# Optimization experiments

Measured on AMD Instinct MI355X. Metric: run time of the kernel, lower is better.

## Reference

```python
import jax, jax.numpy as jnp
import numpy as np

SCALES = [1.0, 0.9, 0.8, 0.7, 0.6]  # [1 - i/10 for i in range(level=5)]
RES_SCALE = 1.0


def conv2d(x, w, b, pad):
    # NCHW conv, OIHW weights, stride 1, symmetric padding
    y = jax.lax.conv_general_dilated(
        x, w, window_strides=(1, 1), padding=[(pad, pad), (pad, pad)],
        dimension_numbers=("NCHW", "OIHW", "NCHW"))
    return y + b[None, :, None, None]


def _cubic_kernel(d, a=-0.75):
    # torch-style bicubic kernel (a = -0.75)
    d = jnp.abs(d)
    w1 = ((a + 2.0) * d - (a + 3.0)) * d * d + 1.0          # |d| <= 1
    w2 = (((a * d) - 5.0 * a) * d + 8.0 * a) * d - 4.0 * a  # 1 < |d| < 2
    return jnp.where(d <= 1.0, w1, jnp.where(d < 2.0, w2, 0.0))


def _resize_axis(x, out_size, axis):
    in_size = x.shape[axis]
    scale = in_size / out_size
    src = (jnp.arange(out_size, dtype=jnp.float32) + 0.5) * scale - 0.5  # align_corners=False
    x0 = jnp.floor(src)
    t = src - x0
    x0 = x0.astype(jnp.int32)
    out = 0.0
    bshape = [1] * x.ndim
    bshape[axis] = out_size
    for off in range(-1, 3):
        idx = jnp.clip(x0 + off, 0, in_size - 1)  # border replicate
        wgt = _cubic_kernel(t - off).reshape(bshape)
        out = out + jnp.take(x, idx, axis=axis) * wgt
    return out


def bicubic(x, oh, ow):
    return _resize_axis(_resize_axis(x, oh, 2), ow, 3)


def setup_inputs() -> dict:
    key = jax.random.key(0)
    ks = jax.random.split(key, 7)
    C, Cr = 64, 32  # channel=64, reduction=2
    x = jax.random.normal(ks[0], (4, C, 48, 48), dtype=jnp.float32)
    wb = jax.random.normal(ks[1], (Cr, C, 3, 3), dtype=jnp.float32) * 0.05  # conv_match_L_base
    bb = jax.random.normal(ks[2], (Cr,), dtype=jnp.float32) * 0.05
    wm = jax.random.normal(ks[3], (Cr, C, 3, 3), dtype=jnp.float32) * 0.05  # conv_match
    bm = jax.random.normal(ks[4], (Cr,), dtype=jnp.float32) * 0.05
    wa = jax.random.normal(ks[5], (C, C, 1, 1), dtype=jnp.float32) * 0.05   # conv_assembly
    ba = jax.random.normal(ks[6], (C,), dtype=jnp.float32) * 0.05
    return {"x": x, "wb": wb, "bb": bb, "wm": wm, "bm": bm, "wa": wa, "ba": ba}


def reference(x, wb, bb, wm, bm, wa, ba):
    N, C, H, W = x.shape
    mb = conv2d(x, wb, bb, 1)                           # [N,Cr,H,W]
    Cr = mb.shape[1]
    mb = mb.reshape(N, Cr, H * W).transpose(0, 2, 1)    # [N,HW,Cr]  (queries)
    raws, keys = [], []
    for s in SCALES:
        ref = x if s == 1.0 else bicubic(x, int(H * s), int(W * s))
        raws.append(conv2d(ref, wa, ba, 0).reshape(N, C, -1))   # values [N,C,HiWi]
        keys.append(conv2d(ref, wm, bm, 1).reshape(N, Cr, -1))  # keys   [N,Cr,HiWi]
    pyr = jnp.concatenate(keys, axis=-1)                        # [N,Cr,L]
    raw = jnp.concatenate(raws, axis=-1).transpose(0, 2, 1)     # [N,L,C]
    score = jax.nn.softmax(jnp.einsum("nqc,ncl->nql", mb, pyr), axis=-1)  # [N,HW,L]
    y = jnp.einsum("nql,nlc->nqc", score, raw)                  # [N,HW,C]
    y = y.transpose(0, 2, 1).reshape(N, C, H, W)
    return y * RES_SCALE + x
```

## Files before the change

### kernel.cpp

```cpp
#include <hip/hip_runtime.h>
#include <math.h>

typedef unsigned short ushort_t;
typedef __attribute__((ext_vector_type(8))) short short8;
typedef __attribute__((ext_vector_type(4))) float float4v;

#define NB 4
#define C 64
#define CR 32
#define HW 2304
#define LTOT 7470
#define LPAD 7472
#define NSEG 15
#define SEG 512
#define LOG2E 1.44269504088896f

#define YP_F 0
#define LP_F 8847360
#define MBBF_F   8985600
#define KEYBF_F  9133056
#define RAWTBF_F 9611136
#define WPK_F    10567552
#define WPQ_F    10576768
#define WPV_F    10585984

static __device__ __forceinline__ ushort_t f2bf(float f) {
  union { float f; unsigned u; } v; v.f = f;
  unsigned r = v.u + 0x7FFF + ((v.u >> 16) & 1);
  return (ushort_t)(r >> 16);
}

__device__ __forceinline__ float cubicw(float d) {
  float ad = fabsf(d);
  float w1 = (1.25f * ad - 2.25f) * ad * ad + 1.0f;
  float w2 = ((-0.75f * ad + 3.75f) * ad - 6.0f) * ad + 3.0f;
  return ad <= 1.0f ? w1 : (ad < 2.0f ? w2 : 0.0f);
}

__global__ void k_zero(ushort_t* __restrict__ xt) {
  int i = blockIdx.x * 256 + threadIdx.x;
  if (i < 264000) {
    uint4 z = {0u, 0u, 0u, 0u};
    *(uint4*)(xt + (size_t)i * 8) = z;
  }
}

__global__ __launch_bounds__(256) void k_pad0(const float* __restrict__ x,
                                              ushort_t* __restrict__ xt) {
  __shared__ float tile[64][49];
  int py = blockIdx.x, n = blockIdx.y, t = threadIdx.x;
#pragma unroll
  for (int i = 0; i < 12; i++) {
    int idx = i * 256 + t;
    int c = idx / 48, px = idx % 48;
    tile[c][px] = x[(size_t)(n * 64 + c) * HW + py * 48 + px];
  }
  __syncthreads();
#pragma unroll
  for (int i = 0; i < 12; i++) {
    int idx = i * 256 + t;
    int c = idx & 63, px = idx >> 6;
    xt[(size_t)(n * 2500 + (py + 1) * 50 + px + 1) * 64 + c] = f2bf(tile[c][px]);
  }
}

__global__ void k_resize(const float* __restrict__ x, ushort_t* __restrict__ xt) {
  int tid = blockIdx.x * 256 + threadIdx.x;
  int D, Dp, PDD, rem, pixb;
  if (tid < 473344)       { D = 43; Dp = 45; PDD = 2025; rem = tid;           pixb = 10000; }
  else if (tid < 843008)  { D = 38; Dp = 40; PDD = 1600; rem = tid - 473344;  pixb = 18100; }
  else if (tid < 1121792) { D = 33; Dp = 35; PDD = 1225; rem = tid - 843008;  pixb = 24500; }
  else                    { D = 28; Dp = 30; PDD = 900;  rem = tid - 1121792; pixb = 29400; }
  int DD = D * D;
  int pix = rem % DD, nc = rem / DD;
  int py = pix / D, px = pix % D;
  float scale = 48.0f / (float)D;
  float sy = ((float)py + 0.5f) * scale - 0.5f;
  float sx = ((float)px + 0.5f) * scale - 0.5f;
  float y0f = floorf(sy), x0f = floorf(sx);
  int y0 = (int)y0f, x0 = (int)x0f;
  float ty = sy - y0f, tx = sx - x0f;
  float wy[4], wxv[4];
#pragma unroll
  for (int k = 0; k < 4; k++) {
    wy[k]  = cubicw(ty - (float)(k - 1));
    wxv[k] = cubicw(tx - (float)(k - 1));
  }
  const float* src = x + (size_t)nc * HW;
  float acc = 0.f;
#pragma unroll
  for (int dy = 0; dy < 4; ++dy) {
    int iy = min(max(y0 - 1 + dy, 0), 47);
    const float* row = src + iy * 48;
    float a = 0.f;
#pragma unroll
    for (int dx = 0; dx < 4; ++dx) {
      int ix = min(max(x0 - 1 + dx, 0), 47);
      a = fmaf(wxv[dx], row[ix], a);
    }
    acc = fmaf(wy[dy], a, acc);
  }
  int n = nc >> 6, c = nc & 63;
  xt[(size_t)(pixb + n * PDD + (py + 1) * Dp + (px + 1)) * 64 + c] = f2bf(acc);
}

__global__ void k_wpack(const float* __restrict__ wm, const float* __restrict__ wb,
                        const float* __restrict__ wa, ushort_t* __restrict__ wpk,
                        ushort_t* __restrict__ wpq, ushort_t* __restrict__ wpv) {
  int tid = blockIdx.x * 256 + threadIdx.x;
  if (tid >= 5120) return;
  int lane = tid & 63, col = lane & 15, kg = lane >> 4;
  if (tid < 4608) {
    int f = (tid >> 6) % 36;
    bool isq = tid >= 2304;
    int tap = f >> 2, half = (f >> 1) & 1, crt = f & 1;
    int cr = crt * 16 + col;
    int ic0 = half * 32 + kg * 8;
    const float* w = isq ? wb : wm;
    short8 v;
#pragma unroll
    for (int j = 0; j < 8; j++) v[j] = (short)f2bf(w[cr * 576 + (ic0 + j) * 9 + tap]);
    *(short8*)((isq ? wpq : wpk) + (size_t)f * 512 + lane * 8) = v;
  } else {
    int id = tid - 4608;
    int f = id >> 6;
    int half = f >> 2, vt = f & 3;
    int c = vt * 16 + col, ic0 = half * 32 + kg * 8;
    short8 v;
#pragma unroll
    for (int j = 0; j < 8; j++) v[j] = (short)f2bf(wa[c * 64 + ic0 + j]);
    *(short8*)(wpv + (size_t)f * 512 + lane * 8) = v;
  }
}

__global__ __launch_bounds__(256) void k_conv(const ushort_t* __restrict__ xt,
    const ushort_t* __restrict__ wpk, const ushort_t* __restrict__ wpq,
    const ushort_t* __restrict__ wpv, const float* __restrict__ bm,
    const float* __restrict__ bb, const float* __restrict__ ba,
    ushort_t* __restrict__ keybf, ushort_t* __restrict__ mbbf,
    ushort_t* __restrict__ rawtbf) {
  int t = threadIdx.x;
  int unit = blockIdx.x * 4 + (t >> 6);
  if (unit >= 938) return;
  int lane = t & 63, col = lane & 15, quad = lane >> 4;
  int n = blockIdx.y;
  int tile = unit >> 1, crt = unit & 1;
  int D, Dp, PDD, DD, pixb, lb, tloc;
  if (tile < 144)      { D = 48; Dp = 50; PDD = 2500; DD = 2304; pixb = 0;     lb = 0;    tloc = tile; }
  else if (tile < 260) { D = 43; Dp = 45; PDD = 2025; DD = 1849; pixb = 10000; lb = 2304; tloc = tile - 144; }
  else if (tile < 351) { D = 38; Dp = 40; PDD = 1600; DD = 1444; pixb = 18100; lb = 4153; tloc = tile - 260; }
  else if (tile < 420) { D = 33; Dp = 35; PDD = 1225; DD = 1089; pixb = 24500; lb = 5597; tloc = tile - 351; }
  else                 { D = 28; Dp = 30; PDD = 900;  DD = 784;  pixb = 29400; lb = 6686; tloc = tile - 420; }
  bool lvl0 = (tile < 144);

  int p = tloc * 16 + col;
  int pv = min(p, DD - 1);
  int py = pv / D, px = pv - py * D;
  const ushort_t* xb = xt + ((size_t)(pixb + n * PDD + (py + 1) * Dp + (px + 1))) * 64 + quad * 8;

  float4v Dk = {0.f, 0.f, 0.f, 0.f};
  float4v Dq = {0.f, 0.f, 0.f, 0.f};
  float4v Dv0 = {0.f, 0.f, 0.f, 0.f};
  float4v Dv1 = {0.f, 0.f, 0.f, 0.f};

#pragma unroll
  for (int dy = -1; dy <= 1; dy++) {
#pragma unroll
    for (int dx = -1; dx <= 1; dx++) {
      int tap = (dy + 1) * 3 + (dx + 1);
      const ushort_t* ab = xb + (dy * Dp + dx) * 64;
#pragma unroll
      for (int half = 0; half < 2; half++) {
        short8 A = *(const short8*)(ab + half * 32);
        int f = (tap * 2 + half) * 2 + crt;
        short8 Bk = *(const short8*)(wpk + (size_t)f * 512 + lane * 8);
        Dk = __builtin_amdgcn_mfma_f32_16x16x32_bf16(A, Bk, Dk, 0, 0, 0);
        if (lvl0) {
          short8 Bq = *(const short8*)(wpq + (size_t)f * 512 + lane * 8);
          Dq = __builtin_amdgcn_mfma_f32_16x16x32_bf16(A, Bq, Dq, 0, 0, 0);
        }
        if (tap == 4) {
          short8 Bv0 = *(const short8*)(wpv + (size_t)(half * 4 + crt * 2) * 512 + lane * 8);
          short8 Bv1 = *(const short8*)(wpv + (size_t)(half * 4 + crt * 2 + 1) * 512 + lane * 8);
          Dv0 = __builtin_amdgcn_mfma_f32_16x16x32_bf16(A, Bv0, Dv0, 0, 0, 0);
          Dv1 = __builtin_amdgcn_mfma_f32_16x16x32_bf16(A, Bv1, Dv1, 0, 0, 0);
        }
      }
    }
  }

  float biask = bm[crt * 16 + col];
  float biasq = bb[crt * 16 + col];
  float biasv0 = ba[crt * 32 + col];
  float biasv1 = ba[crt * 32 + 16 + col];
  int prow = tloc * 16 + quad * 4;
#pragma unroll
  for (int r = 0; r < 4; r++) {
    if (prow + r < DD) {
      int l = lb + prow + r;
      keybf[(size_t)(n * LTOT + l) * 32 + crt * 16 + col] = f2bf(Dk[r] + biask);
      if (lvl0) mbbf[(size_t)(n * HW + l) * 32 + crt * 16 + col] = f2bf((Dq[r] + biasq) * LOG2E);
      rawtbf[(size_t)(n * 64 + crt * 32 + col) * LPAD + l] = f2bf(Dv0[r] + biasv0);
      rawtbf[(size_t)(n * 64 + crt * 32 + 16 + col) * LPAD + l] = f2bf(Dv1[r] + biasv1);
    }
  }
}

__global__ __launch_bounds__(256, 4) void k_attn(const ushort_t* __restrict__ mb,
    const ushort_t* __restrict__ keyb, const ushort_t* __restrict__ rawt,
    float* __restrict__ Yp, float* __restrict__ lp) {
  __shared__ __align__(16) ushort_t VsF[2][4096];
  __shared__ __align__(16) ushort_t Pq[4][32 * 72];

  int t = threadIdx.x;
  int n = blockIdx.y, seg = blockIdx.z;
  int lane = t & 63, wv = t >> 6;
  int col = lane & 15, quad = lane >> 4;
  int qb = blockIdx.x * 128 + wv * 32;
  int l_begin = seg * SEG;
  int l_end = min(l_begin + SEG, LTOT);
  int nfull = (l_end - l_begin) >> 6;
  int rem = (l_end - l_begin) & 63;
  int nch = nfull + (rem ? 1 : 0);

  const ushort_t* keyn = keyb + (size_t)n * LTOT * CR;
  const ushort_t* rawn = rawt + (size_t)n * C * LPAD;

  short8 qA0 = *(const short8*)(mb + ((size_t)(n * HW + qb + col)) * CR + quad * 8);
  short8 qA1 = *(const short8*)(mb + ((size_t)(n * HW + qb + 16 + col)) * CR + quad * 8);

  int ct0 = (t >> 6) & 3, g0 = (t >> 4) & 3, cc0 = t & 15;
  size_t so0 = (size_t)(ct0 * 16 + cc0) * LPAD + g0 * 8;

  float4v Y0[4], Y1[4];
#pragma unroll
  for (int ct = 0; ct < 4; ct++)
#pragma unroll
    for (int r = 0; r < 4; r++) { Y0[ct][r] = 0.f; Y1[ct][r] = 0.f; }
  float ls0 = 0.f, ls1 = 0.f;
  const float4v zero4 = {0.f, 0.f, 0.f, 0.f};
  ushort_t* Pw = Pq[wv];

  uint4 va = *(const uint4*)(rawn + so0 + l_begin);
  uint4 vb = *(const uint4*)(rawn + so0 + 32 + l_begin);
  int buf = 0;

  for (int ch = 0; ch < nch; ++ch) {
    int l0 = l_begin + ch * 64;
    *(uint4*)&VsF[buf][t * 8] = va;
    *(uint4*)&VsF[buf][(t + 256) * 8] = vb;
    if (ch + 1 < nch) {
      int ln = l0 + 64;
      va = *(const uint4*)(rawn + so0 + ln);
      vb = *(const uint4*)(rawn + so0 + 32 + ln);
    }
    __syncthreads();

    bool tail = (rem != 0) && (ch == nfull);
#pragma unroll
    for (int tt = 0; tt < 4; tt++) {
      short8 kf = *(const short8*)(keyn + (size_t)(l0 + tt * 16 + col) * CR + quad * 8);
      float4v S0 = __builtin_amdgcn_mfma_f32_16x16x32_bf16(kf, qA0, zero4, 0, 0, 0);
      float4v S1 = __builtin_amdgcn_mfma_f32_16x16x32_bf16(kf, qA1, zero4, 0, 0, 0);
      int lbase = tt * 16 + quad * 4;
      float p0[4], p1[4];
#pragma unroll
      for (int r = 0; r < 4; r++) {
        bool ok = !tail || (lbase + r < rem);
        float a = __builtin_amdgcn_exp2f(S0[r]);
        float b = __builtin_amdgcn_exp2f(S1[r]);
        p0[r] = ok ? a : 0.f;
        p1[r] = ok ? b : 0.f;
        ls0 += p0[r];
        ls1 += p1[r];
      }
      union { float f; unsigned u; } c0, c1;
      uint2 w;
      c0.f = p0[0]; c1.f = p0[1];
      w.x = ((c0.u + 0x8000u) >> 16) | ((c1.u + 0x8000u) & 0xFFFF0000u);
      c0.f = p0[2]; c1.f = p0[3];
      w.y = ((c0.u + 0x8000u) >> 16) | ((c1.u + 0x8000u) & 0xFFFF0000u);
      *(uint2*)&Pw[col * 72 + lbase] = w;
      c0.f = p1[0]; c1.f = p1[1];
      w.x = ((c0.u + 0x8000u) >> 16) | ((c1.u + 0x8000u) & 0xFFFF0000u);
      c0.f = p1[2]; c1.f = p1[3];
      w.y = ((c0.u + 0x8000u) >> 16) | ((c1.u + 0x8000u) & 0xFFFF0000u);
      *(uint2*)&Pw[(16 + col) * 72 + lbase] = w;
    }

#pragma unroll
    for (int kt = 0; kt < 2; kt++) {
      short8 a0 = *(const short8*)&Pw[col * 72 + kt * 32 + quad * 8];
      short8 a1 = *(const short8*)&Pw[(16 + col) * 72 + kt * 32 + quad * 8];
#pragma unroll
      for (int ct = 0; ct < 4; ct++) {
        short8 bV = *(const short8*)&VsF[buf][(((kt << 2) | ct) * 64 + lane) * 8];
        Y0[ct] = __builtin_amdgcn_mfma_f32_16x16x32_bf16(a0, bV, Y0[ct], 0, 0, 0);
        Y1[ct] = __builtin_amdgcn_mfma_f32_16x16x32_bf16(a1, bV, Y1[ct], 0, 0, 0);
      }
    }
    buf ^= 1;
  }

  ls0 += __shfl_xor(ls0, 16); ls0 += __shfl_xor(ls0, 32);
  ls1 += __shfl_xor(ls1, 16); ls1 += __shfl_xor(ls1, 32);

  float* yo = Yp + ((size_t)(seg * NB + n) * HW + qb) * C;
#pragma unroll
  for (int ct = 0; ct < 4; ct++)
#pragma unroll
    for (int r = 0; r < 4; r++) {
      yo[(quad * 4 + r) * C + ct * 16 + col] = Y0[ct][r];
      yo[(16 + quad * 4 + r) * C + ct * 16 + col] = Y1[ct][r];
    }
  if (quad == 0) {
    int base = (seg * NB + n) * HW + qb;
    lp[base + col] = ls0;
    lp[base + 16 + col] = ls1;
  }
}

__global__ void k_combine(const float* __restrict__ x, const float* __restrict__ ws,
                          float* __restrict__ out) {
  int tid = blockIdx.x * 256 + threadIdx.x;
  int c = tid & 63;
  int t2 = tid >> 6;
  int q = t2 % HW;
  int n = t2 / HW;
  const float* Yv = ws + YP_F;
  const float* lpv = ws + LP_F;
  int i0 = n * HW + q;
  float den = 0.f, num = 0.f;
#pragma unroll
  for (int s = 0; s < NSEG; s++) {
    int idx = s * NB * HW + i0;
    den += lpv[idx];
    num += Yv[(size_t)idx * C + c];
  }
  int oi = (n * C + c) * HW + q;
  out[oi] = num / den + x[oi];
}

extern "C" void kernel_launch(void* const* d_in, const int* in_sizes, int n_in,
                              void* d_out, int out_size, void* d_ws, size_t ws_size,
                              hipStream_t stream) {
  const float* x  = (const float*)d_in[0];
  const float* wb = (const float*)d_in[1];
  const float* bb = (const float*)d_in[2];
  const float* wm = (const float*)d_in[3];
  const float* bm = (const float*)d_in[4];
  const float* wa = (const float*)d_in[5];
  const float* ba = (const float*)d_in[6];
  float* out = (float*)d_out;
  float* ws = (float*)d_ws;
  ushort_t* xt     = (ushort_t*)ws;
  ushort_t* mbbf   = (ushort_t*)(ws + MBBF_F);
  ushort_t* keybf  = (ushort_t*)(ws + KEYBF_F);
  ushort_t* rawtbf = (ushort_t*)(ws + RAWTBF_F);
  ushort_t* wpk    = (ushort_t*)(ws + WPK_F);
  ushort_t* wpq    = (ushort_t*)(ws + WPQ_F);
  ushort_t* wpv    = (ushort_t*)(ws + WPV_F);

  k_zero<<<1032, 256, 0, stream>>>(xt);
  k_pad0<<<dim3(48, 4), 256, 0, stream>>>(x, xt);
  k_resize<<<5166, 256, 0, stream>>>(x, xt);
  k_wpack<<<20, 256, 0, stream>>>(wm, wb, wa, wpk, wpq, wpv);
  k_conv<<<dim3(235, 4), 256, 0, stream>>>(xt, wpk, wpq, wpv, bm, bb, ba,
                                           keybf, mbbf, rawtbf);
  k_attn<<<dim3(18, 4, NSEG), 256, 0, stream>>>(mbbf, keybf, rawtbf,
      ws + YP_F, ws + LP_F);
  k_combine<<<2304, 256, 0, stream>>>(x, ws, out);
}
```

Before: 154.1 us.

## Merge prep kernels and fuse split-L combine into attention via counter

Folds the zero, pad, resize and weight-pack kernels into one prep launch. The prep kernel zeroes only the padding border instead of the whole buffer. The separate combine kernel is removed: each attention block increments a per-(n, query-tile) atomic counter, and the last segment block to arrive reduces the partial outputs and writes the final result with the residual. This cuts launch count and a full zero pass, at the cost of threadfence/atomic ordering and a serial tail in the last-arriving blocks.

```diff
diff --git a/kernel.cpp b/kernel.cpp
--- a/kernel.cpp
+++ b/kernel.cpp
@@ -23,6 +23,7 @@
 #define WPK_F    10567552
 #define WPQ_F    10576768
 #define WPV_F    10585984
+#define CNT_F    10588032
 
 static __device__ __forceinline__ ushort_t f2bf(float f) {
   union { float f; unsigned u; } v; v.f = f;
@@ -37,99 +38,113 @@
   return ad <= 1.0f ? w1 : (ad < 2.0f ? w2 : 0.0f);
 }
 
-__global__ void k_zero(ushort_t* __restrict__ xt) {
-  int i = blockIdx.x * 256 + threadIdx.x;
-  if (i < 264000) {
-    uint4 z = {0u, 0u, 0u, 0u};
-    *(uint4*)(xt + (size_t)i * 8) = z;
-  }
-}
-
-__global__ __launch_bounds__(256) void k_pad0(const float* __restrict__ x,
-                                              ushort_t* __restrict__ xt) {
+__global__ __launch_bounds__(256) void k_prep(const float* __restrict__ x,
+    const float* __restrict__ wm, const float* __restrict__ wb,
+    const float* __restrict__ wa, ushort_t* __restrict__ xt,
+    ushort_t* __restrict__ wpk, ushort_t* __restrict__ wpq,
+    ushort_t* __restrict__ wpv, int* __restrict__ cnt) {
   __shared__ float tile[64][49];
-  int py = blockIdx.x, n = blockIdx.y, t = threadIdx.x;
-#pragma unroll
-  for (int i = 0; i < 12; i++) {
-    int idx = i * 256 + t;
-    int c = idx / 48, px = idx % 48;
-    tile[c][px] = x[(size_t)(n * 64 + c) * HW + py * 48 + px];
-  }
-  __syncthreads();
-#pragma unroll
-  for (int i = 0; i < 12; i++) {
-    int idx = i * 256 + t;
-    int c = idx & 63, px = idx >> 6;
-    xt[(size_t)(n * 2500 + (py + 1) * 50 + px + 1) * 64 + c] = f2bf(tile[c][px]);
-  }
-}
-
-__global__ void k_resize(const float* __restrict__ x, ushort_t* __restrict__ xt) {
-  int tid = blockIdx.x * 256 + threadIdx.x;
-  int D, Dp, PDD, rem, pixb;
-  if (tid < 473344)       { D = 43; Dp = 45; PDD = 2025; rem = tid;           pixb = 10000; }
-  else if (tid < 843008)  { D = 38; Dp = 40; PDD = 1600; rem = tid - 473344;  pixb = 18100; }
-  else if (tid < 1121792) { D = 33; Dp = 35; PDD = 1225; rem = tid - 843008;  pixb = 24500; }
-  else                    { D = 28; Dp = 30; PDD = 900;  rem = tid - 1121792; pixb = 29400; }
-  int DD = D * D;
-  int pix = rem % DD, nc = rem / DD;
-  int py = pix / D, px = pix % D;
-  float scale = 48.0f / (float)D;
-  float sy = ((float)py + 0.5f) * scale - 0.5f;
-  float sx = ((float)px + 0.5f) * scale - 0.5f;
-  float y0f = floorf(sy), x0f = floorf(sx);
-  int y0 = (int)y0f, x0 = (int)x0f;
-  float ty = sy - y0f, tx = sx - x0f;
-  float wy[4], wxv[4];
-#pragma unroll
-  for (int k = 0; k < 4; k++) {
-    wy[k]  = cubicw(ty - (float)(k - 1));
-    wxv[k] = cubicw(tx - (float)(k - 1));
-  }
-  const float* src = x + (size_t)nc * HW;
-  float acc = 0.f;
-#pragma unroll
-  for (int dy = 0; dy < 4; ++dy) {
-    int iy = min(max(y0 - 1 + dy, 0), 47);
-    const float* row = src + iy * 48;
-    float a = 0.f;
-#pragma unroll
-    for (int dx = 0; dx < 4; ++dx) {
-      int ix = min(max(x0 - 1 + dx, 0), 47);
-      a = fmaf(wxv[dx], row[ix], a);
-    }
-    acc = fmaf(wy[dy], a, acc);
-  }
-  int n = nc >> 6, c = nc & 63;
-  xt[(size_t)(pixb + n * PDD + (py + 1) * Dp + (px + 1)) * 64 + c] = f2bf(acc);
-}
-
-__global__ void k_wpack(const float* __restrict__ wm, const float* __restrict__ wb,
-                        const float* __restrict__ wa, ushort_t* __restrict__ wpk,
-                        ushort_t* __restrict__ wpq, ushort_t* __restrict__ wpv) {
-  int tid = blockIdx.x * 256 + threadIdx.x;
-  if (tid >= 5120) return;
-  int lane = tid & 63, col = lane & 15, kg = lane >> 4;
-  if (tid < 4608) {
-    int f = (tid >> 6) % 36;
-    bool isq = tid >= 2304;
-    int tap = f >> 2, half = (f >> 1) & 1, crt = f & 1;
-    int cr = crt * 16 + col;
-    int ic0 = half * 32 + kg * 8;
-    const float* w = isq ? wb : wm;
-    short8 v;
-#pragma unroll
-    for (int j = 0; j < 8; j++) v[j] = (short)f2bf(w[cr * 576 + (ic0 + j) * 9 + tap]);
-    *(short8*)((isq ? wpq : wpk) + (size_t)f * 512 + lane * 8) = v;
+  int bx = blockIdx.x, t = threadIdx.x;
+
+  if (bx < 98) {
+    int item = bx * 256 + t;
+    if (item < 24960) {
+      int pxslot = item >> 3, c8 = item & 7;
+      int n = pxslot / 780, rr = pxslot % 780;
+      int Dp, PDD, pixb, r;
+      if (rr < 196)      { Dp = 50; PDD = 2500; pixb = 0;     r = rr; }
+      else if (rr < 372) { Dp = 45; PDD = 2025; pixb = 10000; r = rr - 196; }
+      else if (rr < 528) { Dp = 40; PDD = 1600; pixb = 18100; r = rr - 372; }
+      else if (rr < 664) { Dp = 35; PDD = 1225; pixb = 24500; r = rr - 528; }
+      else               { Dp = 30; PDD = 900;  pixb = 29400; r = rr - 664; }
+      int py, px;
+      if (r < Dp)            { py = 0; px = r; }
+      else if (r < 2 * Dp)   { py = Dp - 1; px = r - Dp; }
+      else { int s = r - 2 * Dp; py = 1 + (s >> 1); px = (s & 1) ? Dp - 1 : 0; }
+      uint4 z = {0u, 0u, 0u, 0u};
+      *(uint4*)(xt + ((size_t)(pixb + n * PDD + py * Dp + px)) * 64 + c8 * 8) = z;
+    }
+    if (bx == 97 && t >= 128 && t < 200) cnt[t - 128] = 0;
+  } else if (bx < 290) {
+    int pb = bx - 98;
+    int py = pb % 48, n = pb / 48;
+#pragma unroll
+    for (int i = 0; i < 12; i++) {
+      int idx = i * 256 + t;
+      int c = idx / 48, px = idx % 48;
+      tile[c][px] = x[(size_t)(n * 64 + c) * HW + py * 48 + px];
+    }
+    __syncthreads();
+#pragma unroll
+    for (int i = 0; i < 12; i++) {
+      int idx = i * 256 + t;
+      int c = idx & 63, px = idx >> 6;
+      xt[(size_t)(n * 2500 + (py + 1) * 50 + px + 1) * 64 + c] = f2bf(tile[c][px]);
+    }
+  } else if (bx < 5456) {
+    int tid = (bx - 290) * 256 + t;
+    if (tid >= 1322496) return;
+    int D, Dp, PDD, rem, pixb;
+    if (tid < 473344)       { D = 43; Dp = 45; PDD = 2025; rem = tid;           pixb = 10000; }
+    else if (tid < 843008)  { D = 38; Dp = 40; PDD = 1600; rem = tid - 473344;  pixb = 18100; }
+    else if (tid < 1121792) { D = 33; Dp = 35; PDD = 1225; rem = tid - 843008;  pixb = 24500; }
+    else                    { D = 28; Dp = 30; PDD = 900;  rem = tid - 1121792; pixb = 29400; }
+    int DD = D * D;
+    int pix = rem % DD, nc = rem / DD;
+    int py = pix / D, px = pix % D;
+    float scale = 48.0f / (float)D;
+    float sy = ((float)py + 0.5f) * scale - 0.5f;
+    float sx = ((float)px + 0.5f) * scale - 0.5f;
+    float y0f = floorf(sy), x0f = floorf(sx);
+    int y0 = (int)y0f, x0 = (int)x0f;
+    float ty = sy - y0f, tx = sx - x0f;
+    float wy[4], wxv[4];
+#pragma unroll
+    for (int k = 0; k < 4; k++) {
+      wy[k]  = cubicw(ty - (float)(k - 1));
+      wxv[k] = cubicw(tx - (float)(k - 1));
+    }
+    const float* src = x + (size_t)nc * HW;
+    float acc = 0.f;
+#pragma unroll
+    for (int dy = 0; dy < 4; ++dy) {
+      int iy = min(max(y0 - 1 + dy, 0), 47);
+      const float* row = src + iy * 48;
+      float a = 0.f;
+#pragma unroll
+      for (int dx = 0; dx < 4; ++dx) {
+        int ix = min(max(x0 - 1 + dx, 0), 47);
+        a = fmaf(wxv[dx], row[ix], a);
+      }
+      acc = fmaf(wy[dy], a, acc);
+    }
+    int n = nc >> 6, c = nc & 63;
+    xt[(size_t)(pixb + n * PDD + (py + 1) * Dp + (px + 1)) * 64 + c] = f2bf(acc);
   } else {
-    int id = tid - 4608;
-    int f = id >> 6;
-    int half = f >> 2, vt = f & 3;
-    int c = vt * 16 + col, ic0 = half * 32 + kg * 8;
-    short8 v;
-#pragma unroll
-    for (int j = 0; j < 8; j++) v[j] = (short)f2bf(wa[c * 64 + ic0 + j]);
-    *(short8*)(wpv + (size_t)f * 512 + lane * 8) = v;
+    int tid = (bx - 5456) * 256 + t;
+    if (tid >= 5120) return;
+    int lane = tid & 63, col = lane & 15, kg = lane >> 4;
+    if (tid < 4608) {
+      int f = (tid >> 6) % 36;
+      bool isq = tid >= 2304;
+      int tap = f >> 2, half = (f >> 1) & 1, crt = f & 1;
+      int cr = crt * 16 + col;
+      int ic0 = half * 32 + kg * 8;
+      const float* w = isq ? wb : wm;
+      short8 v;
+#pragma unroll
+      for (int j = 0; j < 8; j++) v[j] = (short)f2bf(w[cr * 576 + (ic0 + j) * 9 + tap]);
+      *(short8*)((isq ? wpq : wpk) + (size_t)f * 512 + lane * 8) = v;
+    } else {
+      int id = tid - 4608;
+      int f = id >> 6;
+      int half = f >> 2, vt = f & 3;
+      int c = vt * 16 + col, ic0 = half * 32 + kg * 8;
+      short8 v;
+#pragma unroll
+      for (int j = 0; j < 8; j++) v[j] = (short)f2bf(wa[c * 64 + ic0 + j]);
+      *(short8*)(wpv + (size_t)f * 512 + lane * 8) = v;
+    }
   }
 }
 
@@ -208,9 +223,11 @@
 
 __global__ __launch_bounds__(256, 4) void k_attn(const ushort_t* __restrict__ mb,
     const ushort_t* __restrict__ keyb, const ushort_t* __restrict__ rawt,
-    float* __restrict__ Yp, float* __restrict__ lp) {
+    const float* __restrict__ x, float* __restrict__ Yp, float* __restrict__ lp,
+    int* __restrict__ cnt, float* __restrict__ out) {
   __shared__ __align__(16) ushort_t VsF[2][4096];
   __shared__ __align__(16) ushort_t Pq[4][32 * 72];
+  __shared__ int isLast;
 
   int t = threadIdx.x;
   int n = blockIdx.y, seg = blockIdx.z;
@@ -318,27 +335,37 @@
     lp[base + col] = ls0;
     lp[base + 16 + col] = ls1;
   }
-}
-
-__global__ void k_combine(const float* __restrict__ x, const float* __restrict__ ws,
-                          float* __restrict__ out) {
-  int tid = blockIdx.x * 256 + threadIdx.x;
-  int c = tid & 63;
-  int t2 = tid >> 6;
-  int q = t2 % HW;
-  int n = t2 / HW;
-  const float* Yv = ws + YP_F;
-  const float* lpv = ws + LP_F;
-  int i0 = n * HW + q;
-  float den = 0.f, num = 0.f;
-#pragma unroll
-  for (int s = 0; s < NSEG; s++) {
-    int idx = s * NB * HW + i0;
-    den += lpv[idx];
-    num += Yv[(size_t)idx * C + c];
-  }
-  int oi = (n * C + c) * HW + q;
-  out[oi] = num / den + x[oi];
+
+  __threadfence();
+  if (t == 0) {
+    int old = atomicAdd(&cnt[n * 18 + blockIdx.x], 1);
+    isLast = (old == NSEG - 1);
+  }
+  __syncthreads();
+  if (!isLast) return;
+  __threadfence();
+
+  int qb0 = blockIdx.x * 128;
+#pragma unroll
+  for (int i = 0; i < 8; i++) {
+    int slot = t + i * 256;
+    int q = slot >> 4, c4 = slot & 15;
+    int gq = qb0 + q;
+    float nx = 0.f, ny = 0.f, nz = 0.f, nw = 0.f, den = 0.f;
+#pragma unroll 5
+    for (int s = 0; s < NSEG; s++) {
+      int base = (s * NB + n) * HW + gq;
+      const float* yv = Yp + (size_t)base * C + c4 * 4;
+      nx += yv[0]; ny += yv[1]; nz += yv[2]; nw += yv[3];
+      den += lp[base];
+    }
+    float inv = 1.0f / den;
+    int ob = (n * C + c4 * 4) * HW + gq;
+    out[ob]          = nx * inv + x[ob];
+    out[ob + HW]     = ny * inv + x[ob + HW];
+    out[ob + 2 * HW] = nz * inv + x[ob + 2 * HW];
+    out[ob + 3 * HW] = nw * inv + x[ob + 3 * HW];
+  }
 }
 
 extern "C" void kernel_launch(void* const* d_in, const int* in_sizes, int n_in,
@@ -360,14 +387,11 @@
   ushort_t* wpk    = (ushort_t*)(ws + WPK_F);
   ushort_t* wpq    = (ushort_t*)(ws + WPQ_F);
   ushort_t* wpv    = (ushort_t*)(ws + WPV_F);
-
-  k_zero<<<1032, 256, 0, stream>>>(xt);
-  k_pad0<<<dim3(48, 4), 256, 0, stream>>>(x, xt);
-  k_resize<<<5166, 256, 0, stream>>>(x, xt);
-  k_wpack<<<20, 256, 0, stream>>>(wm, wb, wa, wpk, wpq, wpv);
+  int* cnt         = (int*)(ws + CNT_F);
+
+  k_prep<<<5476, 256, 0, stream>>>(x, wm, wb, wa, xt, wpk, wpq, wpv, cnt);
   k_conv<<<dim3(235, 4), 256, 0, stream>>>(xt, wpk, wpq, wpv, bm, bb, ba,
                                            keybf, mbbf, rawtbf);
-  k_attn<<<dim3(18, 4, NSEG), 256, 0, stream>>>(mbbf, keybf, rawtbf,
-      ws + YP_F, ws + LP_F);
-  k_combine<<<2304, 256, 0, stream>>>(x, ws, out);
-}
+  k_attn<<<dim3(18, 4, NSEG), 256, 0, stream>>>(mbbf, keybf, rawtbf, x,
+      ws + YP_F, ws + LP_F, cnt, out);
+}
```

Result: slower. 295.8 us (+92.0%).
